# Optimization experiments

Hardware: AMD Instinct MI355X
Metric: run time of the kernel (lower is better)

Reference implementation:

```python
import jax, jax.numpy as jnp
import numpy as np

B, C, Z, E = 2, 32, 4, 2
N = C * C * Z  # 4096 grid points per element
P_TH, T_TH = 0.5, 0.5
ELE_D = (0.74, 0.528)


def _consts():
    real_size = jnp.array([25.0, 25.0, 3.0], jnp.float32)
    lattice = real_size / jnp.array([C, C, Z], jnp.float32)
    g = jnp.stack(jnp.meshgrid(jnp.arange(C), jnp.arange(C), jnp.arange(Z), indexing='ij'), axis=-1)
    pit = g.reshape(N, 3).astype(jnp.float32)
    return pit, lattice


def _cdist(a, b):
    # a [M,3], b [K,3] -> [M,K] euclidean distance
    d2 = jnp.sum((a[:, None, :] - b[None, :, :]) ** 2, axis=-1)
    return jnp.sqrt(d2)


def _nms(pos, conf, valid, ele_d):
    # Fixed-shape version of Analyzer.nms: sort by confidence desc (invalid -> -inf, sorts last),
    # triu(<d) adjacency restricted to valid points, matrix-multiply suppression correction.
    key = jnp.where(valid, conf, -jnp.inf)
    order = jnp.argsort(-key)              # descending confidence
    pos_s = pos[order]
    valid_s = valid[order]
    dist = _cdist(pos_s, pos_s)            # [N,N] ~ 64 MB
    iu = jnp.triu(jnp.ones((N, N), bool), k=1)
    adj = ((dist < ele_d) & iu & valid_s[:, None] & valid_s[None, :]).astype(pos.dtype)
    restrain = adj.sum(0)                  # col sums: # earlier neighbors
    restrain_one = (restrain != 0).astype(pos.dtype)
    correct = restrain_one @ adj           # earlier neighbors that are themselves suppressed
    sel = ((restrain - correct) == 0) & valid_s
    keep = jnp.zeros(N, bool).at[order].set(sel)
    return keep & valid


def _match(t_pos, t_valid, p_pos, p_valid, ele_d):
    # TP matching: T point is matched if any valid P within ele_d; argmin gives its P partner.
    dist = _cdist(t_pos, p_pos)            # [N,N]
    dist = jnp.where(t_valid[:, None] & p_valid[None, :], dist, jnp.inf)
    tp_t_mask = (dist < ele_d).any(1)      # rows in torch's TP_T_index
    tp_p_idx = jnp.argmin(dist, axis=1).astype(jnp.int32)  # torch's TP_P_index (valid where tp_t_mask)
    return tp_t_mask, tp_p_idx


def setup_inputs() -> dict:
    key = jax.random.key(0)
    k1, k2 = jax.random.split(key)
    predictions = jax.random.uniform(k1, (B, C, C, Z, E, 4), jnp.float32)
    targets = jax.random.uniform(k2, (B, C, C, Z, E, 4), jnp.float32)
    return {"predictions": predictions, "targets": targets}


def reference(predictions, targets):
    pit, lattice = _consts()
    # [B,C,C,Z,E,4] -> [B,E,N,4]
    pred = predictions.reshape(B, C, C, Z, E, 4).transpose(0, 4, 1, 2, 3, 5).reshape(B, E, N, 4)
    tgt = targets.reshape(B, C, C, Z, E, 4).transpose(0, 4, 1, 2, 3, 5).reshape(B, E, N, 4)

    p_pos = (pred[..., :3] + pit) * lattice    # [B,E,N,3] absolute coords
    p_conf = pred[..., 3]
    mask_p = p_conf > P_TH
    t_pos = (tgt[..., :3] + pit) * lattice
    mask_t = tgt[..., 3] > T_TH

    keeps, tpt, tpp, tptn, tppn = [], [], [], [], []
    for e in range(E):
        d = ELE_D[e]
        keep_e = jax.vmap(lambda p, c, v: _nms(p, c, v, d))(p_pos[:, e], p_conf[:, e], mask_p[:, e])
        tt, tp = jax.vmap(lambda tq, tv, pq, pv: _match(tq, tv, pq, pv, d))(
            t_pos[:, e], mask_t[:, e], p_pos[:, e], mask_p[:, e])
        ttn, tpn = jax.vmap(lambda tq, tv, pq, pv: _match(tq, tv, pq, pv, d))(
            t_pos[:, e], mask_t[:, e], p_pos[:, e], keep_e)
        keeps.append(keep_e); tpt.append(tt); tpp.append(tp); tptn.append(ttn); tppn.append(tpn)

    keep_nms = jnp.stack(keeps, 1)   # [B,E,N] combined mask_p & nms keep
    tp_t_mask = jnp.stack(tpt, 1)
    tp_p_idx = jnp.stack(tpp, 1)
    tp_t_mask_nms = jnp.stack(tptn, 1)
    tp_p_idx_nms = jnp.stack(tppn, 1)

    return (p_pos, mask_p, keep_nms, t_pos, mask_t,
            tp_t_mask, tp_p_idx, tp_t_mask_nms, tp_p_idx_nms)
```

## Files before the change

### kernel.cpp

```cpp
#include <hip/hip_runtime.h>
#include <cmath>
#include <cstdint>

namespace {
constexpr int NPT  = 4096;
constexpr int NTOT = 16384;

constexpr int O_PPOS  = 0;
constexpr int O_MASKP = 49152;
constexpr int O_KEEP  = 65536;
constexpr int O_TPOS  = 81920;
constexpr int O_MASKT = 131072;
constexpr int O_TPT   = 147456;
constexpr int O_TPP   = 163840;
constexpr int O_TPTN  = 180224;
constexpr int O_TPPN  = 196608;

constexpr size_t W_RESTR = 0;
constexpr size_t W_KEEP  = 16384;
constexpr size_t W_CNT   = 32768;
constexpr size_t W_LIST  = 33024;

constexpr float GUARD = 1.4999f;
}

__device__ __forceinline__ unsigned long long shfl_xor_u64(unsigned long long v, int m) {
    unsigned lo = (unsigned)v, hi = (unsigned)(v >> 32);
    lo = __shfl_xor(lo, m); hi = __shfl_xor(hi, m);
    return ((unsigned long long)hi << 32) | lo;
}
__device__ __forceinline__ unsigned long long shfl_down_u64(unsigned long long v, int m) {
    unsigned lo = (unsigned)v, hi = (unsigned)(v >> 32);
    lo = __shfl_down(lo, m); hi = __shfl_down(hi, m);
    return ((unsigned long long)hi << 32) | lo;
}

__device__ __forceinline__ float3 cellpos(float4 p, int n) {
#pragma clang fp contract(off)
    float fx = (float)(n >> 7), fy = (float)((n >> 2) & 31), fz = (float)(n & 3);
    float3 r;
    r.x = (p.x + fx) * 0.78125f;
    r.y = (p.y + fy) * 0.78125f;
    r.z = (p.z + fz) * 0.75f;
    return r;
}
__device__ __forceinline__ float dist2(float3 a, float3 b) {
#pragma clang fp contract(off)
    float dx = a.x - b.x, dy = a.y - b.y, dz = a.z - b.z;
    float d2 = dx * dx + dy * dy;
    return d2 + dz * dz;
}

__global__ void __launch_bounds__(256) k_restrain(const float4* __restrict__ pred,
                                                  float* __restrict__ out,
                                                  unsigned char* __restrict__ restru,
                                                  unsigned* __restrict__ cnt,
                                                  float s0, float s1) {
#pragma clang fp contract(off)
    int tid = blockIdx.x * 256 + threadIdx.x;
    if (tid == 0) *cnt = 0u;
    int row = tid >> 1, h = tid & 1;
    int n = row & (NPT - 1), s = row >> 12, b = s >> 1, e = s & 1;
    int base4 = b * 8192 + e;
    float se = (s & 1) ? s1 : s0;
    float4 p = pred[base4 + n * 2];
    float3 pj = cellpos(p, n);
    bool valid = p.w > 0.5f;
    if (h == 0) {
        out[O_PPOS + row * 3 + 0] = pj.x;
        out[O_PPOS + row * 3 + 1] = pj.y;
        out[O_PPOS + row * 3 + 2] = pj.z;
        out[O_MASKP + row] = valid ? 1.0f : 0.0f;
    }
    unsigned c = 0;
    if (valid) {
        int gx = n >> 7, gy = (n >> 2) & 31;
        for (int qq = 0; qq < 5; ++qq) {
            int q = qq * 2 + h;
            if (q > 8) continue;
            int nx = gx + q / 3 - 1, ny = gy + q % 3 - 1;
            if ((unsigned)nx > 31u || (unsigned)ny > 31u) continue;
            int nb = nx * 128 + ny * 4;
#pragma unroll
            for (int nz = 0; nz < 4; ++nz) {
                int ni = nb + nz;
                float4 pi = pred[base4 + ni * 2];
                float3 qi = cellpos(pi, ni);
                float d2 = dist2(pj, qi);
                bool prec = (pi.w > p.w) || ((pi.w == p.w) && (ni < n));
                if ((pi.w > 0.5f) && (d2 < se) && prec) c++;
            }
        }
    }
    c += __shfl_xor(c, 1);
    if (h == 0) restru[row] = (unsigned char)c;
}

__global__ void __launch_bounds__(256) k_suppress(const float4* __restrict__ pred,
                                                  const unsigned char* __restrict__ restru,
                                                  float* __restrict__ out,
                                                  unsigned char* __restrict__ keepu,
                                                  float s0, float s1) {
#pragma clang fp contract(off)
    int tid = blockIdx.x * 256 + threadIdx.x;
    int row = tid >> 1, h = tid & 1;
    int n = row & (NPT - 1), s = row >> 12, b = s >> 1, e = s & 1;
    int base4 = b * 8192 + e, srow = s * NPT;
    float se = (s & 1) ? s1 : s0;
    float4 p = pred[base4 + n * 2];
    float3 pj = cellpos(p, n);
    bool valid = p.w > 0.5f;
    unsigned any = 0;
    if (valid) {
        int gx = n >> 7, gy = (n >> 2) & 31;
        for (int qq = 0; qq < 5; ++qq) {
            int q = qq * 2 + h;
            if (q > 8) continue;
            int nx = gx + q / 3 - 1, ny = gy + q % 3 - 1;
            if ((unsigned)nx > 31u || (unsigned)ny > 31u) continue;
            int nb = nx * 128 + ny * 4;
#pragma unroll
            for (int nz = 0; nz < 4; ++nz) {
                int ni = nb + nz;
                float4 pi = pred[base4 + ni * 2];
                float3 qi = cellpos(pi, ni);
                float d2 = dist2(pj, qi);
                bool prec = (pi.w > p.w) || ((pi.w == p.w) && (ni < n));
                bool flg = (pi.w > 0.5f) && (restru[srow + ni] == 0);
                if (flg && (d2 < se) && prec) any = 1u;
            }
        }
    }
    any |= __shfl_xor(any, 1);
    if (h == 0) {
        bool keep = valid && !any;
        out[O_KEEP + row] = keep ? 1.0f : 0.0f;
        keepu[row] = keep ? 1 : 0;
    }
}

__global__ void __launch_bounds__(256) k_match1(const float4* __restrict__ pred,
                                                const float4* __restrict__ tgt,
                                                const unsigned char* __restrict__ keepu,
                                                float* __restrict__ out,
                                                unsigned* __restrict__ list,
                                                unsigned* __restrict__ cnt,
                                                float s0, float s1) {
#pragma clang fp contract(off)
    int tid = blockIdx.x * 256 + threadIdx.x;
    int row = tid >> 2, h = tid & 3;
    int n = row & (NPT - 1), s = row >> 12, b = s >> 1, e = s & 1;
    int base4 = b * 8192 + e, srow = s * NPT;
    float se = (s & 1) ? s1 : s0;
    float4 t4 = tgt[base4 + n * 2];
    float3 tj = cellpos(t4, n);
    bool tv = t4.w > 0.5f;
    if (h == 0) {
        out[O_TPOS + row * 3 + 0] = tj.x;
        out[O_TPOS + row * 3 + 1] = tj.y;
        out[O_TPOS + row * 3 + 2] = tj.z;
        out[O_MASKT + row] = tv ? 1.0f : 0.0f;
    }
    if (!tv) {
        if (h == 0) {
            out[O_TPT + row] = 0.0f; out[O_TPTN + row] = 0.0f;
            out[O_TPP + row] = 0.0f; out[O_TPPN + row] = 0.0f;
        }
        return;
    }
    int gx = n >> 7, gy = (n >> 2) & 31;
    unsigned long long bs = ~0ull, bn = ~0ull;
    unsigned as_ = 0, an_ = 0;
    for (int qq = 0; qq < 7; ++qq) {
        int q = qq * 4 + h;
        if (q > 24) continue;
        int nx = gx + q / 5 - 2, ny = gy + q % 5 - 2;
        if ((unsigned)nx > 31u || (unsigned)ny > 31u) continue;
        int nb = nx * 128 + ny * 4;
#pragma unroll
        for (int nz = 0; nz < 4; ++nz) {
            int ni = nb + nz;
            float4 pi = pred[base4 + ni * 2];
            float3 qi = cellpos(pi, ni);
            float d2 = dist2(tj, qi);
            float dist = sqrtf(d2);
            unsigned long long enc =
                ((unsigned long long)__float_as_uint(dist) << 32) | (unsigned)ni;
            if (pi.w > 0.5f) { if (enc < bs) bs = enc; if (d2 < se) as_ = 1u; }
            if (keepu[srow + ni]) { if (enc < bn) bn = enc; if (d2 < se) an_ = 1u; }
        }
    }
    for (int m = 1; m < 4; m <<= 1) {
        unsigned long long o = shfl_xor_u64(bs, m); if (o < bs) bs = o;
        o = shfl_xor_u64(bn, m); if (o < bn) bn = o;
        as_ |= __shfl_xor(as_, m);
        an_ |= __shfl_xor(an_, m);
    }
    if (h == 0) {
        out[O_TPT + row]  = as_ ? 1.0f : 0.0f;
        out[O_TPTN + row] = an_ ? 1.0f : 0.0f;
        bool acc_s = __uint_as_float((unsigned)(bs >> 32)) < GUARD;
        bool acc_n = __uint_as_float((unsigned)(bn >> 32)) < GUARD;
        if (acc_s) out[O_TPP + row]  = (float)(unsigned)(bs & 0xffffffffull);
        if (acc_n) out[O_TPPN + row] = (float)(unsigned)(bn & 0xffffffffull);
        if (!acc_s || !acc_n) list[atomicAdd(cnt, 1u)] = (unsigned)row;
    }
}

__global__ void __launch_bounds__(256) k_match2(const float4* __restrict__ pred,
                                                const float4* __restrict__ tgt,
                                                const unsigned char* __restrict__ keepu,
                                                const unsigned* __restrict__ list,
                                                const unsigned* __restrict__ cnt,
                                                float* __restrict__ out) {
#pragma clang fp contract(off)
    __shared__ unsigned long long rs[4], rn[4];
    unsigned C = *cnt;
    for (unsigned r = blockIdx.x; r < C; r += gridDim.x) {
        int row = (int)list[r];
        int n = row & (NPT - 1), s = row >> 12, b = s >> 1, e = s & 1;
        int base4 = b * 8192 + e, srow = s * NPT;
        float4 t4 = tgt[base4 + n * 2];
        float3 tj = cellpos(t4, n);
        unsigned long long bs = ~0ull, bn = ~0ull;
        for (int k = (int)threadIdx.x; k < NPT; k += 256) {
            float4 pi = pred[base4 + k * 2];
            float3 qi = cellpos(pi, k);
            float d2 = dist2(tj, qi);
            float dist = sqrtf(d2);
            unsigned long long enc =
                ((unsigned long long)__float_as_uint(dist) << 32) | (unsigned)k;
            if (pi.w > 0.5f && enc < bs) bs = enc;
            if (keepu[srow + k] && enc < bn) bn = enc;
        }
        for (int m = 32; m; m >>= 1) {
            unsigned long long o = shfl_down_u64(bs, m); if (o < bs) bs = o;
            o = shfl_down_u64(bn, m); if (o < bn) bn = o;
        }
        int w = (int)(threadIdx.x >> 6);
        if ((threadIdx.x & 63) == 0) { rs[w] = bs; rn[w] = bn; }
        __syncthreads();
        if (threadIdx.x == 0) {
            for (int i = 1; i < 4; ++i) {
                if (rs[i] < bs) bs = rs[i];
                if (rn[i] < bn) bn = rn[i];
            }
            unsigned is_ = (bs == ~0ull) ? 0u : (unsigned)(bs & 0xffffffffull);
            unsigned in_ = (bn == ~0ull) ? 0u : (unsigned)(bn & 0xffffffffull);
            out[O_TPP + row]  = (float)is_;
            out[O_TPPN + row] = (float)in_;
        }
        __syncthreads();
    }
}

static float sq_boundary(float t) {
    float f = (float)((double)t * (double)t);
    while (sqrtf(f) >= t) f = nextafterf(f, 0.0f);
    while (sqrtf(f) < t)  f = nextafterf(f, __builtin_inff());
    return f;
}

extern "C" void kernel_launch(void* const* d_in, const int* in_sizes, int n_in,
                              void* d_out, int out_size, void* d_ws, size_t ws_size,
                              hipStream_t stream) {
    (void)in_sizes; (void)n_in; (void)out_size; (void)ws_size;
    const float4* pred = (const float4*)d_in[0];
    const float4* tgt  = (const float4*)d_in[1];
    float* out = (float*)d_out;
    char* ws = (char*)d_ws;

    unsigned char* restru = (unsigned char*)(ws + W_RESTR);
    unsigned char* keepu  = (unsigned char*)(ws + W_KEEP);
    unsigned* cnt  = (unsigned*)(ws + W_CNT);
    unsigned* list = (unsigned*)(ws + W_LIST);

    float s0 = sq_boundary(0.74f);
    float s1 = sq_boundary(0.528f);

    k_restrain<<<dim3(128), dim3(256), 0, stream>>>(pred, out, restru, cnt, s0, s1);
    k_suppress<<<dim3(128), dim3(256), 0, stream>>>(pred, restru, out, keepu, s0, s1);
    k_match1 <<<dim3(256), dim3(256), 0, stream>>>(pred, tgt, keepu, out, list, cnt, s0, s1);
    k_match2 <<<dim3(128), dim3(256), 0, stream>>>(pred, tgt, keepu, list, cnt, out);
}
```

Before: 78.69 us.

## Fuse NMS restrain/suppress via shared-memory halo; inline match fallback scan

The restrain and suppress passes become one kernel in which each block loads a six-column halo of precomputed positions into shared memory, computes restrain counts for the interior plus a one-column halo, and then evaluates suppression locally. The aim is to drop a kernel launch and repeated global gathers. The two match kernels are also merged: rows whose local-window result is not guaranteed exact now rescan all 4096 points inside the same four-lane group, instead of being appended to a list for a block-wide second kernel. This removes the atomic list and one launch, but any fallback rows become long serial scans across only four lanes, which could stall whole waves.

```diff
diff --git a/kernel.cpp b/kernel.cpp
--- a/kernel.cpp
+++ b/kernel.cpp
@@ -4,7 +4,6 @@
 
 namespace {
 constexpr int NPT  = 4096;
-constexpr int NTOT = 16384;
 
 constexpr int O_PPOS  = 0;
 constexpr int O_MASKP = 49152;
@@ -16,22 +15,12 @@
 constexpr int O_TPTN  = 180224;
 constexpr int O_TPPN  = 196608;
 
-constexpr size_t W_RESTR = 0;
-constexpr size_t W_KEEP  = 16384;
-constexpr size_t W_CNT   = 32768;
-constexpr size_t W_LIST  = 33024;
-
 constexpr float GUARD = 1.4999f;
 }
 
 __device__ __forceinline__ unsigned long long shfl_xor_u64(unsigned long long v, int m) {
     unsigned lo = (unsigned)v, hi = (unsigned)(v >> 32);
     lo = __shfl_xor(lo, m); hi = __shfl_xor(hi, m);
-    return ((unsigned long long)hi << 32) | lo;
-}
-__device__ __forceinline__ unsigned long long shfl_down_u64(unsigned long long v, int m) {
-    unsigned lo = (unsigned)v, hi = (unsigned)(v >> 32);
-    lo = __shfl_down(lo, m); hi = __shfl_down(hi, m);
     return ((unsigned long long)hi << 32) | lo;
 }
 
@@ -44,110 +33,116 @@
     r.z = (p.z + fz) * 0.75f;
     return r;
 }
-__device__ __forceinline__ float dist2(float3 a, float3 b) {
+__device__ __forceinline__ float dist2v(float4 a, float4 b) {
 #pragma clang fp contract(off)
     float dx = a.x - b.x, dy = a.y - b.y, dz = a.z - b.z;
     float d2 = dx * dx + dy * dy;
     return d2 + dz * dz;
 }
-
-__global__ void __launch_bounds__(256) k_restrain(const float4* __restrict__ pred,
-                                                  float* __restrict__ out,
-                                                  unsigned char* __restrict__ restru,
-                                                  unsigned* __restrict__ cnt,
-                                                  float s0, float s1) {
-#pragma clang fp contract(off)
-    int tid = blockIdx.x * 256 + threadIdx.x;
-    if (tid == 0) *cnt = 0u;
-    int row = tid >> 1, h = tid & 1;
-    int n = row & (NPT - 1), s = row >> 12, b = s >> 1, e = s & 1;
+__device__ __forceinline__ float dist2f(float3 a, float3 b) {
+#pragma clang fp contract(off)
+    float dx = a.x - b.x, dy = a.y - b.y, dz = a.z - b.z;
+    float d2 = dx * dx + dy * dy;
+    return d2 + dz * dz;
+}
+
+__global__ void __launch_bounds__(256) k_nms(const float4* __restrict__ pred,
+                                             float* __restrict__ out,
+                                             unsigned char* __restrict__ keepu,
+                                             float s0, float s1) {
+#pragma clang fp contract(off)
+    __shared__ float4 pw[6][128];
+    __shared__ unsigned char rsh[4][128];
+    int bid = blockIdx.x;
+    int s = bid >> 4, gx0 = (bid & 15) * 2;
+    int b = s >> 1, e = s & 1;
     int base4 = b * 8192 + e;
     float se = (s & 1) ? s1 : s0;
-    float4 p = pred[base4 + n * 2];
-    float3 pj = cellpos(p, n);
-    bool valid = p.w > 0.5f;
-    if (h == 0) {
-        out[O_PPOS + row * 3 + 0] = pj.x;
-        out[O_PPOS + row * 3 + 1] = pj.y;
-        out[O_PPOS + row * 3 + 2] = pj.z;
-        out[O_MASKP + row] = valid ? 1.0f : 0.0f;
-    }
-    unsigned c = 0;
+
+    for (int idx = (int)threadIdx.x; idx < 768; idx += 256) {
+        int p = idx >> 7, r = idx & 127;
+        int gx = gx0 - 2 + p;
+        float4 v = make_float4(0.f, 0.f, 0.f, -1.0f);
+        if ((unsigned)gx <= 31u) {
+            int n = gx * 128 + r;
+            float4 raw = pred[base4 + n * 2];
+            float3 q = cellpos(raw, n);
+            v = make_float4(q.x, q.y, q.z, raw.w > 0.5f ? raw.w : -1.0f);
+        }
+        pw[p][r] = v;
+    }
+    __syncthreads();
+
+    for (int ii = 0; ii < 2; ++ii) {
+        int idx = (int)threadIdx.x + ii * 256;
+        int p2 = idx >> 7, r = idx & 127;
+        int gx = gx0 - 1 + p2, gy = r >> 2;
+        float4 pj = pw[p2 + 1][r];
+        unsigned c = 0;
+        if (pj.w > 0.0f && (unsigned)gx <= 31u) {
+            int n = gx * 128 + r;
+            for (int dx = -1; dx <= 1; ++dx) {
+                for (int dy = -1; dy <= 1; ++dy) {
+                    int ny = gy + dy;
+                    if ((unsigned)ny > 31u) continue;
+#pragma unroll
+                    for (int nz = 0; nz < 4; ++nz) {
+                        int rr = ny * 4 + nz;
+                        float4 pi = pw[p2 + 1 + dx][rr];
+                        int ni = (gx + dx) * 128 + rr;
+                        float d2 = dist2v(pj, pi);
+                        bool prec = (pi.w > pj.w) || ((pi.w == pj.w) && (ni < n));
+                        if ((pi.w > 0.0f) && (d2 < se) && prec) c++;
+                    }
+                }
+            }
+        }
+        rsh[p2][r] = (unsigned char)c;
+    }
+    __syncthreads();
+
+    int t = (int)threadIdx.x;
+    int pg = t >> 7, r = t & 127;
+    int gx = gx0 + pg, gy = r >> 2;
+    int n = gx * 128 + r;
+    int row = s * NPT + n;
+    float4 pj = pw[pg + 2][r];
+    out[O_PPOS + row * 3 + 0] = pj.x;
+    out[O_PPOS + row * 3 + 1] = pj.y;
+    out[O_PPOS + row * 3 + 2] = pj.z;
+    bool valid = pj.w > 0.0f;
+    out[O_MASKP + row] = valid ? 1.0f : 0.0f;
+    bool sup = false;
     if (valid) {
-        int gx = n >> 7, gy = (n >> 2) & 31;
-        for (int qq = 0; qq < 5; ++qq) {
-            int q = qq * 2 + h;
-            if (q > 8) continue;
-            int nx = gx + q / 3 - 1, ny = gy + q % 3 - 1;
-            if ((unsigned)nx > 31u || (unsigned)ny > 31u) continue;
-            int nb = nx * 128 + ny * 4;
+        for (int dx = -1; dx <= 1; ++dx) {
+            for (int dy = -1; dy <= 1; ++dy) {
+                int ny = gy + dy;
+                if ((unsigned)ny > 31u) continue;
 #pragma unroll
-            for (int nz = 0; nz < 4; ++nz) {
-                int ni = nb + nz;
-                float4 pi = pred[base4 + ni * 2];
-                float3 qi = cellpos(pi, ni);
-                float d2 = dist2(pj, qi);
-                bool prec = (pi.w > p.w) || ((pi.w == p.w) && (ni < n));
-                if ((pi.w > 0.5f) && (d2 < se) && prec) c++;
+                for (int nz = 0; nz < 4; ++nz) {
+                    int rr = ny * 4 + nz;
+                    float4 pi = pw[pg + 2 + dx][rr];
+                    int ni = (gx + dx) * 128 + rr;
+                    float d2 = dist2v(pj, pi);
+                    bool prec = (pi.w > pj.w) || ((pi.w == pj.w) && (ni < n));
+                    bool flg = (pi.w > 0.0f) && (rsh[pg + 1 + dx][rr] == 0);
+                    sup = sup || (flg && (d2 < se) && prec);
+                }
             }
         }
     }
-    c += __shfl_xor(c, 1);
-    if (h == 0) restru[row] = (unsigned char)c;
-}
-
-__global__ void __launch_bounds__(256) k_suppress(const float4* __restrict__ pred,
-                                                  const unsigned char* __restrict__ restru,
-                                                  float* __restrict__ out,
-                                                  unsigned char* __restrict__ keepu,
-                                                  float s0, float s1) {
-#pragma clang fp contract(off)
-    int tid = blockIdx.x * 256 + threadIdx.x;
-    int row = tid >> 1, h = tid & 1;
-    int n = row & (NPT - 1), s = row >> 12, b = s >> 1, e = s & 1;
-    int base4 = b * 8192 + e, srow = s * NPT;
-    float se = (s & 1) ? s1 : s0;
-    float4 p = pred[base4 + n * 2];
-    float3 pj = cellpos(p, n);
-    bool valid = p.w > 0.5f;
-    unsigned any = 0;
-    if (valid) {
-        int gx = n >> 7, gy = (n >> 2) & 31;
-        for (int qq = 0; qq < 5; ++qq) {
-            int q = qq * 2 + h;
-            if (q > 8) continue;
-            int nx = gx + q / 3 - 1, ny = gy + q % 3 - 1;
-            if ((unsigned)nx > 31u || (unsigned)ny > 31u) continue;
-            int nb = nx * 128 + ny * 4;
-#pragma unroll
-            for (int nz = 0; nz < 4; ++nz) {
-                int ni = nb + nz;
-                float4 pi = pred[base4 + ni * 2];
-                float3 qi = cellpos(pi, ni);
-                float d2 = dist2(pj, qi);
-                bool prec = (pi.w > p.w) || ((pi.w == p.w) && (ni < n));
-                bool flg = (pi.w > 0.5f) && (restru[srow + ni] == 0);
-                if (flg && (d2 < se) && prec) any = 1u;
-            }
-        }
-    }
-    any |= __shfl_xor(any, 1);
-    if (h == 0) {
-        bool keep = valid && !any;
-        out[O_KEEP + row] = keep ? 1.0f : 0.0f;
-        keepu[row] = keep ? 1 : 0;
-    }
-}
-
-__global__ void __launch_bounds__(256) k_match1(const float4* __restrict__ pred,
-                                                const float4* __restrict__ tgt,
-                                                const unsigned char* __restrict__ keepu,
-                                                float* __restrict__ out,
-                                                unsigned* __restrict__ list,
-                                                unsigned* __restrict__ cnt,
-                                                float s0, float s1) {
-#pragma clang fp contract(off)
-    int tid = blockIdx.x * 256 + threadIdx.x;
+    bool keep = valid && !sup;
+    out[O_KEEP + row] = keep ? 1.0f : 0.0f;
+    keepu[row] = keep ? 1 : 0;
+}
+
+__global__ void __launch_bounds__(256) k_match(const float4* __restrict__ pred,
+                                               const float4* __restrict__ tgt,
+                                               const unsigned char* __restrict__ keepu,
+                                               float* __restrict__ out,
+                                               float s0, float s1) {
+#pragma clang fp contract(off)
+    int tid = blockIdx.x * 256 + (int)threadIdx.x;
     int row = tid >> 2, h = tid & 3;
     int n = row & (NPT - 1), s = row >> 12, b = s >> 1, e = s & 1;
     int base4 = b * 8192 + e, srow = s * NPT;
@@ -182,7 +177,7 @@
             int ni = nb + nz;
             float4 pi = pred[base4 + ni * 2];
             float3 qi = cellpos(pi, ni);
-            float d2 = dist2(tj, qi);
+            float d2 = dist2f(tj, qi);
             float dist = sqrtf(d2);
             unsigned long long enc =
                 ((unsigned long long)__float_as_uint(dist) << 32) | (unsigned)ni;
@@ -199,58 +194,37 @@
     if (h == 0) {
         out[O_TPT + row]  = as_ ? 1.0f : 0.0f;
         out[O_TPTN + row] = an_ ? 1.0f : 0.0f;
-        bool acc_s = __uint_as_float((unsigned)(bs >> 32)) < GUARD;
-        bool acc_n = __uint_as_float((unsigned)(bn >> 32)) < GUARD;
-        if (acc_s) out[O_TPP + row]  = (float)(unsigned)(bs & 0xffffffffull);
-        if (acc_n) out[O_TPPN + row] = (float)(unsigned)(bn & 0xffffffffull);
-        if (!acc_s || !acc_n) list[atomicAdd(cnt, 1u)] = (unsigned)row;
-    }
-}
-
-__global__ void __launch_bounds__(256) k_match2(const float4* __restrict__ pred,
-                                                const float4* __restrict__ tgt,
-                                                const unsigned char* __restrict__ keepu,
-                                                const unsigned* __restrict__ list,
-                                                const unsigned* __restrict__ cnt,
-                                                float* __restrict__ out) {
-#pragma clang fp contract(off)
-    __shared__ unsigned long long rs[4], rn[4];
-    unsigned C = *cnt;
-    for (unsigned r = blockIdx.x; r < C; r += gridDim.x) {
-        int row = (int)list[r];
-        int n = row & (NPT - 1), s = row >> 12, b = s >> 1, e = s & 1;
-        int base4 = b * 8192 + e, srow = s * NPT;
-        float4 t4 = tgt[base4 + n * 2];
-        float3 tj = cellpos(t4, n);
-        unsigned long long bs = ~0ull, bn = ~0ull;
-        for (int k = (int)threadIdx.x; k < NPT; k += 256) {
-            float4 pi = pred[base4 + k * 2];
-            float3 qi = cellpos(pi, k);
-            float d2 = dist2(tj, qi);
-            float dist = sqrtf(d2);
-            unsigned long long enc =
-                ((unsigned long long)__float_as_uint(dist) << 32) | (unsigned)k;
-            if (pi.w > 0.5f && enc < bs) bs = enc;
-            if (keepu[srow + k] && enc < bn) bn = enc;
-        }
-        for (int m = 32; m; m >>= 1) {
-            unsigned long long o = shfl_down_u64(bs, m); if (o < bs) bs = o;
-            o = shfl_down_u64(bn, m); if (o < bn) bn = o;
-        }
-        int w = (int)(threadIdx.x >> 6);
-        if ((threadIdx.x & 63) == 0) { rs[w] = bs; rn[w] = bn; }
-        __syncthreads();
-        if (threadIdx.x == 0) {
-            for (int i = 1; i < 4; ++i) {
-                if (rs[i] < bs) bs = rs[i];
-                if (rn[i] < bn) bn = rn[i];
-            }
-            unsigned is_ = (bs == ~0ull) ? 0u : (unsigned)(bs & 0xffffffffull);
-            unsigned in_ = (bn == ~0ull) ? 0u : (unsigned)(bn & 0xffffffffull);
-            out[O_TPP + row]  = (float)is_;
-            out[O_TPPN + row] = (float)in_;
-        }
-        __syncthreads();
+    }
+    bool acc_s = __uint_as_float((unsigned)(bs >> 32)) < GUARD;
+    bool acc_n = __uint_as_float((unsigned)(bn >> 32)) < GUARD;
+    if (acc_s && acc_n) {
+        if (h == 0) {
+            out[O_TPP + row]  = (float)(unsigned)(bs & 0xffffffffull);
+            out[O_TPPN + row] = (float)(unsigned)(bn & 0xffffffffull);
+        }
+        return;
+    }
+    bs = ~0ull; bn = ~0ull;
+#pragma unroll 4
+    for (int k = h; k < NPT; k += 4) {
+        float4 pi = pred[base4 + k * 2];
+        float3 qi = cellpos(pi, k);
+        float d2 = dist2f(tj, qi);
+        float dist = sqrtf(d2);
+        unsigned long long enc =
+            ((unsigned long long)__float_as_uint(dist) << 32) | (unsigned)k;
+        if (pi.w > 0.5f && enc < bs) bs = enc;
+        if (keepu[srow + k] && enc < bn) bn = enc;
+    }
+    for (int m = 1; m < 4; m <<= 1) {
+        unsigned long long o = shfl_xor_u64(bs, m); if (o < bs) bs = o;
+        o = shfl_xor_u64(bn, m); if (o < bn) bn = o;
+    }
+    if (h == 0) {
+        unsigned is_ = (bs == ~0ull) ? 0u : (unsigned)(bs & 0xffffffffull);
+        unsigned in_ = (bn == ~0ull) ? 0u : (unsigned)(bn & 0xffffffffull);
+        out[O_TPP + row]  = (float)is_;
+        out[O_TPPN + row] = (float)in_;
     }
 }
 
@@ -268,18 +242,11 @@
     const float4* pred = (const float4*)d_in[0];
     const float4* tgt  = (const float4*)d_in[1];
     float* out = (float*)d_out;
-    char* ws = (char*)d_ws;
-
-    unsigned char* restru = (unsigned char*)(ws + W_RESTR);
-    unsigned char* keepu  = (unsigned char*)(ws + W_KEEP);
-    unsigned* cnt  = (unsigned*)(ws + W_CNT);
-    unsigned* list = (unsigned*)(ws + W_LIST);
+    unsigned char* keepu = (unsigned char*)d_ws;
 
     float s0 = sq_boundary(0.74f);
     float s1 = sq_boundary(0.528f);
 
-    k_restrain<<<dim3(128), dim3(256), 0, stream>>>(pred, out, restru, cnt, s0, s1);
-    k_suppress<<<dim3(128), dim3(256), 0, stream>>>(pred, restru, out, keepu, s0, s1);
-    k_match1 <<<dim3(256), dim3(256), 0, stream>>>(pred, tgt, keepu, out, list, cnt, s0, s1);
-    k_match2 <<<dim3(128), dim3(256), 0, stream>>>(pred, tgt, keepu, list, cnt, out);
-}
+    k_nms  <<<dim3(64),  dim3(256), 0, stream>>>(pred, out, keepu, s0, s1);
+    k_match<<<dim3(256), dim3(256), 0, stream>>>(pred, tgt, keepu, out, s0, s1);
+}
```

After: 79.96 us. No clear change (+1.6%).
